# Kernel optimization log

Hardware: AMD Instinct MI355X
Metric: run time of the kernel (lower is better)

The kernel has to match this reference:

```python
import jax, jax.numpy as jnp
import numpy as np

TEMPERATURE = 0.1  # init kwarg
EPS = 1e-8        # torch cosine_similarity eps


def setup_inputs() -> dict:
    key = jax.random.key(0)
    k1, k2, k3 = jax.random.split(key, 3)
    B, D, C = 4096, 1024, 32
    representations = jax.random.normal(k1, (B, D), dtype=jnp.float32)
    soft_labels = jax.random.uniform(k2, (B, C), dtype=jnp.float32)
    labels = jax.random.randint(k3, (B,), 0, 32, dtype=jnp.int64)
    return {
        "representations": representations,
        "soft_labels": soft_labels,
        "labels": labels,
        "pseudo_weight": 10,
    }


def reference(representations, soft_labels, labels, pseudo_weight):
    B = representations.shape[0]
    # row-normalize (cosine similarity)
    norms = jnp.maximum(jnp.linalg.norm(representations, axis=1, keepdims=True), EPS)
    rn = representations / norms
    Z = (rn @ rn.T) / TEMPERATURE                      # [B, B] scaled cosine sims
    E = jnp.exp(Z)
    off_diag = 1.0 - jnp.eye(B, dtype=Z.dtype)         # exclude j == i
    denom = jnp.sum(E * off_diag, axis=1, keepdims=True)   # [B, 1]
    loss_arr = -(Z - jnp.log(denom))                   # -log(exp(Z_ij)/denom_i)
    # positive-pair weights: same label, j != i (detached in original)
    pos = (labels[:, None] == labels[None, :]).astype(Z.dtype) * off_diag
    soft_sim = jax.lax.stop_gradient(soft_labels @ soft_labels.T)  # torch.inner, detached
    w = pos + pseudo_weight * soft_sim
    return jnp.sum(loss_arr * w) / B
```

## Files before the change

kernel.cpp:

```cpp
#include <hip/hip_runtime.h>
#include <hip/hip_bf16.h>
#include <stdint.h>


typedef float f32x4 __attribute__((ext_vector_type(4)));
typedef long i64;

#define INV_T 10.0f
#define Z_SCALE (INV_T / 256.0f)

#define CHUNK_STRIDE 262144

#define GLD16(gp, lp)                                                          \
    __builtin_amdgcn_global_load_lds(                                          \
        (const __attribute__((address_space(1))) uint32_t*)(gp),               \
        (__attribute__((address_space(3))) uint32_t*)(lp), 16, 0, 0)

#define OFF_RNF8  0
#define OFF_DENOM 4194304
#define OFF_POSS  (OFF_DENOM + 16384)
#define OFF_G     (OFF_POSS + 16384)
#define OFF_OACC  (OFF_G + 131072)
#define OFF_DONE  (OFF_OACC + 16)
#define ZERO_SPAN 167936
#define OFF_CSP   (OFF_DENOM + ZERO_SPAN)
#define OFF_CCP   (OFF_CSP + 4096)
#define OFF_W     (OFF_CCP + 4096)

#define N_GEMM 528
#define N_G    512
#define N_W    16

__global__ __launch_bounds__(256) void scl_stage1(const float* __restrict__ rep,
                                                  const float* __restrict__ sl,
                                                  const int* __restrict__ labels,
                                                  uint8_t* __restrict__ rnf8,
                                                  float* __restrict__ cs_part,
                                                  int* __restrict__ cc_part,
                                                  char* __restrict__ zbase) {
    int b = blockIdx.x;
    int t = threadIdx.x;
    if (b < 4096) {
        int row = b;
        const float4* src = reinterpret_cast<const float4*>(rep + (size_t)row * 1024);
        float4 v = src[t];
        float s = v.x * v.x + v.y * v.y + v.z * v.z + v.w * v.w;
#pragma unroll
        for (int m = 1; m < 64; m <<= 1) s += __shfl_xor(s, m, 64);
        __shared__ float red[4];
        if ((t & 63) == 0) red[t >> 6] = s;
        __syncthreads();
        s = red[0] + red[1] + red[2] + red[3];
        float nf = 16.0f / fmaxf(sqrtf(s), 1e-8f);
        int p = 0;
        p = __builtin_amdgcn_cvt_pk_fp8_f32(v.x * nf, v.y * nf, p, false);
        p = __builtin_amdgcn_cvt_pk_fp8_f32(v.z * nf, v.w * nf, p, true);
        *(uint32_t*)&rnf8[(size_t)(t >> 4) * CHUNK_STRIDE + row * 64 + (t & 15) * 4] =
            (uint32_t)p;
    } else if (b < 4128) {
        __shared__ float part[8][32];
        __shared__ int bins[32];
        int bb = b - 4096;
        if (t < 32) bins[t] = 0;
        __syncthreads();
        if (t < 128) atomicAdd(&bins[labels[bb * 128 + t]], 1);
        int c = t & 31, rg = t >> 5;
        float s = 0.f;
#pragma unroll 4
        for (int k = 0; k < 16; ++k) {
            int i = bb * 128 + rg * 16 + k;
            s += sl[i * 32 + c];
        }
        part[rg][c] = s;
        __syncthreads();
        if (t < 32) {
            float tot = 0.f;
#pragma unroll
            for (int g = 0; g < 8; ++g) tot += part[g][t];
            cs_part[bb * 32 + t] = tot;
            cc_part[bb * 32 + t] = bins[t];
        }
    } else {
        int zb = b - 4128;
        *(uint4*)(zbase + (size_t)zb * 4096 + t * 16) = (uint4){0, 0, 0, 0};
    }
}

__global__ __launch_bounds__(256) void scl_gw(const uint8_t* __restrict__ rnf8,
                                              const float* __restrict__ sl,
                                              const int* __restrict__ labels,
                                              const float* __restrict__ cs_part,
                                              const int* __restrict__ cc_part,
                                              const int* __restrict__ pwp,
                                              float* __restrict__ G,
                                              float* __restrict__ W) {
    int tid = threadIdx.x;
    int bIdx = blockIdx.x;

    if (bIdx < N_G) {
        __shared__ __align__(16) uint8_t rns[128 * 64];
        __shared__ __align__(16) float sls[128 * 32];
        int dblk = bIdx & 15, ks = bIdx >> 4;
        int i0 = ks * 128;
        const uint8_t* slab = rnf8 + (size_t)dblk * CHUNK_STRIDE + (size_t)i0 * 64;
#pragma unroll
        for (int p = 0; p < 2; ++p) {
            int off = p * 4096 + tid * 16;
            *(uint4*)&rns[off] = *(const uint4*)&slab[off];
        }
#pragma unroll
        for (int p = 0; p < 4; ++p) {
            int off = p * 1024 + tid * 4;
            *(float4*)&sls[off] = *(const float4*)&sl[(size_t)i0 * 32 + off];
        }
        __syncthreads();
        int dq = tid >> 5, c = tid & 31;
        int d0 = dblk * 64 + dq * 8;
        float acc[8];
#pragma unroll
        for (int j = 0; j < 8; ++j) acc[j] = 0.f;
#pragma unroll 4
        for (int k = 0; k < 128; ++k) {
            uint2 rv = *(const uint2*)&rns[k * 64 + dq * 8];
            float sv = sls[k * 32 + c];
            acc[0] += __builtin_amdgcn_cvt_f32_fp8((int)rv.x, 0) * sv;
            acc[1] += __builtin_amdgcn_cvt_f32_fp8((int)rv.x, 1) * sv;
            acc[2] += __builtin_amdgcn_cvt_f32_fp8((int)rv.x, 2) * sv;
            acc[3] += __builtin_amdgcn_cvt_f32_fp8((int)rv.x, 3) * sv;
            acc[4] += __builtin_amdgcn_cvt_f32_fp8((int)rv.y, 0) * sv;
            acc[5] += __builtin_amdgcn_cvt_f32_fp8((int)rv.y, 1) * sv;
            acc[6] += __builtin_amdgcn_cvt_f32_fp8((int)rv.y, 2) * sv;
            acc[7] += __builtin_amdgcn_cvt_f32_fp8((int)rv.y, 3) * sv;
        }
#pragma unroll
        for (int j = 0; j < 8; ++j)
            atomicAdd(&G[(d0 + j) * 32 + c], acc[j] * 0.0625f);
    } else {
        __shared__ __align__(16) float css[32];
        __shared__ int ccs[32];
        if (tid < 32) {
            float s = 0.f; int n = 0;
#pragma unroll
            for (int b = 0; b < 32; ++b) { s += cs_part[b * 32 + tid]; n += cc_part[b * 32 + tid]; }
            css[tid] = s; ccs[tid] = n;
        }
        __syncthreads();
        int bits = *pwp;
        float pw = (bits >= -(1 << 22) && bits <= (1 << 22)) ? (float)bits
                                                             : __int_as_float(bits);
        int i = (bIdx - N_G) * 256 + tid;
        const f32x4* sl4 = (const f32x4*)sl;
        const f32x4* cs4 = (const f32x4*)css;
        float dW = 0.f;
#pragma unroll
        for (int q = 0; q < 8; ++q) {
            f32x4 s = sl4[i * 8 + q];
            f32x4 c = cs4[q];
            dW += s[0] * c[0] + s[1] * c[1] + s[2] * c[2] + s[3] * c[3];
        }
        W[i] = (float)(ccs[labels[i]] - 1) + pw * dW;
    }
}

__global__ __launch_bounds__(256) void scl_gemm(const uint8_t* __restrict__ rnf8,
                                                const int* __restrict__ labels,
                                                float* __restrict__ denom,
                                                float* __restrict__ posS) {
    int tid = threadIdx.x;
    int bIdx = blockIdx.x;

    __shared__ __align__(16) uint8_t As[3][128 * 64];
    __shared__ __align__(16) uint8_t Bs[3][128 * 64];
    __shared__ int lblA[128], lblB[128];

    int L = (bIdx & 7) * 66 + (bIdx >> 3);
    int bi = 0, rem = L;
    while (rem >= 32 - bi) { rem -= 32 - bi; ++bi; }
    int bj = bi + rem;
    int rowA0 = bi * 128, colB0 = bj * 128;

    if (tid < 128) {
        lblA[tid] = labels[rowA0 + tid];
        lblB[tid] = labels[colB0 + tid];
    }

    int lane = tid & 63, warp = tid >> 6;
    int wr = warp >> 1, wc = warp & 1;
    int m_ = lane & 15, g = lane >> 4;

    int r4 = lane >> 2;
    int csw = (lane & 3) ^ ((lane >> 3) & 3);
    const uint8_t* gA0 = rnf8 + (size_t)(rowA0 + warp * 32 + r4) * 64 + csw * 16;
    const uint8_t* gB0 = rnf8 + (size_t)(colB0 + warp * 32 + r4) * 64 + csw * 16;

    f32x4 acc[4][4];
#pragma unroll
    for (int a = 0; a < 4; ++a)
#pragma unroll
        for (int b = 0; b < 4; ++b) acc[a][b] = (f32x4){0.f, 0.f, 0.f, 0.f};

    int fsw = (g ^ ((m_ >> 1) & 3)) * 16;

    GLD16(gA0,                     &As[0][(warp * 32) * 64]);
    GLD16(gA0 + 1024,              &As[0][(warp * 32 + 16) * 64]);
    GLD16(gB0,                     &Bs[0][(warp * 32) * 64]);
    GLD16(gB0 + 1024,              &Bs[0][(warp * 32 + 16) * 64]);
    GLD16(gA0 + CHUNK_STRIDE,        &As[1][(warp * 32) * 64]);
    GLD16(gA0 + CHUNK_STRIDE + 1024, &As[1][(warp * 32 + 16) * 64]);
    GLD16(gB0 + CHUNK_STRIDE,        &Bs[1][(warp * 32) * 64]);
    GLD16(gB0 + CHUNK_STRIDE + 1024, &Bs[1][(warp * 32 + 16) * 64]);

    asm volatile("s_waitcnt lgkmcnt(0)" ::: "memory");

    for (int kt = 0; kt < 15; ++kt) {
        int cur = kt % 3;
        asm volatile("s_waitcnt vmcnt(4)" ::: "memory");
        __builtin_amdgcn_s_barrier();
        __builtin_amdgcn_sched_barrier(0);
        f32x4 aq[4], bq[4];
#pragma unroll
        for (int ti = 0; ti < 4; ++ti) {
            int rowLoc = wr * 64 + ti * 16 + m_;
            aq[ti] = *(const f32x4*)&As[cur][rowLoc * 64 + fsw];
        }
#pragma unroll
        for (int tj = 0; tj < 4; ++tj) {
            int colLoc = wc * 64 + tj * 16 + m_;
            bq[tj] = *(const f32x4*)&Bs[cur][colLoc * 64 + fsw];
        }
        if (kt < 14) {
            int nxt = (kt + 2) % 3;
            size_t co = (size_t)(kt + 2) * CHUNK_STRIDE;
            GLD16(gA0 + co,        &As[nxt][(warp * 32) * 64]);
            GLD16(gA0 + co + 1024, &As[nxt][(warp * 32 + 16) * 64]);
            GLD16(gB0 + co,        &Bs[nxt][(warp * 32) * 64]);
            GLD16(gB0 + co + 1024, &Bs[nxt][(warp * 32 + 16) * 64]);
        }
#pragma unroll
        for (int s = 0; s < 2; ++s)
#pragma unroll
            for (int ti = 0; ti < 4; ++ti)
#pragma unroll
                for (int tj = 0; tj < 4; ++tj) {
                    i64 a = ((const i64*)&aq[ti])[s];
                    i64 b = ((const i64*)&bq[tj])[s];
                    acc[ti][tj] = __builtin_amdgcn_mfma_f32_16x16x32_fp8_fp8(
                        a, b, acc[ti][tj], 0, 0, 0);
                }
    }
    {
        int cur = 15 % 3;
        asm volatile("s_waitcnt vmcnt(0)" ::: "memory");
        __builtin_amdgcn_s_barrier();
        __builtin_amdgcn_sched_barrier(0);
        f32x4 aq[4], bq[4];
#pragma unroll
        for (int ti = 0; ti < 4; ++ti) {
            int rowLoc = wr * 64 + ti * 16 + m_;
            aq[ti] = *(const f32x4*)&As[cur][rowLoc * 64 + fsw];
        }
#pragma unroll
        for (int tj = 0; tj < 4; ++tj) {
            int colLoc = wc * 64 + tj * 16 + m_;
            bq[tj] = *(const f32x4*)&Bs[cur][colLoc * 64 + fsw];
        }
#pragma unroll
        for (int s = 0; s < 2; ++s)
#pragma unroll
            for (int ti = 0; ti < 4; ++ti)
#pragma unroll
                for (int tj = 0; tj < 4; ++tj) {
                    i64 a = ((const i64*)&aq[ti])[s];
                    i64 b = ((const i64*)&bq[tj])[s];
                    acc[ti][tj] = __builtin_amdgcn_mfma_f32_16x16x32_fp8_fp8(
                        a, b, acc[ti][tj], 0, 0, 0);
                }
    }

    bool isDiag = (bi == bj);
    int cl = m_;
    float colE[4] = {0.f, 0.f, 0.f, 0.f}, colP[4] = {0.f, 0.f, 0.f, 0.f};
#pragma unroll
    for (int ti = 0; ti < 4; ++ti) {
        int rowLoc = wr * 64 + ti * 16 + g * 4;
        float rE[4] = {0.f, 0.f, 0.f, 0.f}, rP[4] = {0.f, 0.f, 0.f, 0.f};
        int lr[4];
#pragma unroll
        for (int r = 0; r < 4; ++r) lr[r] = lblA[rowLoc + r];
#pragma unroll
        for (int tj = 0; tj < 4; ++tj) {
            int colLoc = wc * 64 + tj * 16 + cl;
            int gCol = colB0 + colLoc;
            int lc = lblB[colLoc];
            f32x4 a = acc[ti][tj];
#pragma unroll
            for (int r = 0; r < 4; ++r) {
                int gRow = rowA0 + rowLoc + r;
                float z = Z_SCALE * a[r];
                float e = __expf(z);
                bool offd = (gRow != gCol);
                if (!offd) e = 0.f;
                rE[r] += e;
                colE[tj] += e;
                if (offd && (lr[r] == lc)) { rP[r] += z; colP[tj] += z; }
            }
        }
#pragma unroll
        for (int r = 0; r < 4; ++r) {
            float v = rE[r], p = rP[r];
#pragma unroll
            for (int msk = 1; msk < 16; msk <<= 1) {
                v += __shfl_xor(v, msk, 64);
                p += __shfl_xor(p, msk, 64);
            }
            if (cl == 0) {
                int gRow = rowA0 + rowLoc + r;
                atomicAdd(&denom[gRow], v);
                atomicAdd(&posS[gRow], p);
            }
        }
    }
    if (!isDiag) {
#pragma unroll
        for (int tj = 0; tj < 4; ++tj) {
            float v = colE[tj], p = colP[tj];
            v += __shfl_xor(v, 16, 64); p += __shfl_xor(p, 16, 64);
            v += __shfl_xor(v, 32, 64); p += __shfl_xor(p, 32, 64);
            if (g == 0) {
                int gCol = colB0 + wc * 64 + tj * 16 + cl;
                atomicAdd(&denom[gCol], v);
                atomicAdd(&posS[gCol], p);
            }
        }
    }
}

__global__ __launch_bounds__(256) void scl_finalize(const float* __restrict__ denom,
                                                    const float* __restrict__ posS,
                                                    const float* __restrict__ W,
                                                    const float* __restrict__ G,
                                                    const int* __restrict__ pwp,
                                                    double* __restrict__ oacc,
                                                    int* __restrict__ done,
                                                    float* __restrict__ out) {
    int t = threadIdx.x;
    __shared__ double wsum[4];
    double contrib = 0.0;

    if (blockIdx.x < 8) {
        int i0 = blockIdx.x * 512 + t;
        float t0 = __logf(denom[i0]) * W[i0] - posS[i0];
        float t1 = __logf(denom[i0 + 256]) * W[i0 + 256] - posS[i0 + 256];
        double td = (double)t0 + (double)t1;
#pragma unroll
        for (int m = 1; m < 64; m <<= 1) td += __shfl_xor(td, m, 64);
        if ((t & 63) == 0) wsum[t >> 6] = td;
        __syncthreads();
        contrib = wsum[0] + wsum[1] + wsum[2] + wsum[3];
    } else {
        int bits = *pwp;
        float pw = (bits >= -(1 << 22) && bits <= (1 << 22)) ? (float)bits
                                                             : __int_as_float(bits);
        const f32x4* G4 = (const f32x4*)G;
        float gs = 0.f;
#pragma unroll
        for (int q = 0; q < 32; ++q) {
            f32x4 v = G4[q * 256 + t];
            gs += v[0] * v[0] + v[1] * v[1] + v[2] * v[2] + v[3] * v[3];
        }
        double gd = (double)gs;
#pragma unroll
        for (int m = 1; m < 64; m <<= 1) gd += __shfl_xor(gd, m, 64);
        if ((t & 63) == 0) wsum[t >> 6] = gd;
        __syncthreads();
        contrib = -(double)(pw * INV_T) * (wsum[0] + wsum[1] + wsum[2] + wsum[3]);
    }

    if (t == 0) {
        atomicAdd(oacc, contrib);
        __threadfence();
        int old = atomicAdd(done, 1);
        if (old == 8) {
            double tot = atomicAdd(oacc, 0.0);
            out[0] = (float)(tot * (1.0 / 4096.0));
        }
    }
}

extern "C" void kernel_launch(void* const* d_in, const int* in_sizes, int n_in,
                              void* d_out, int out_size, void* d_ws, size_t ws_size,
                              hipStream_t stream) {
    const float* rep = (const float*)d_in[0];
    const float* sl = (const float*)d_in[1];
    const int* labels = (const int*)d_in[2];
    const int* pwp = (const int*)d_in[3];

    char* ws = (char*)d_ws;
    uint8_t* rnf8 = (uint8_t*)(ws + OFF_RNF8);
    float* denom = (float*)(ws + OFF_DENOM);
    float* posS = (float*)(ws + OFF_POSS);
    float* G = (float*)(ws + OFF_G);
    double* oacc = (double*)(ws + OFF_OACC);
    int* done = (int*)(ws + OFF_DONE);
    float* cs_part = (float*)(ws + OFF_CSP);
    int* cc_part = (int*)(ws + OFF_CCP);
    float* W = (float*)(ws + OFF_W);

    scl_stage1<<<4169, 256, 0, stream>>>(rep, sl, labels, rnf8,
                                         cs_part, cc_part, ws + OFF_DENOM);
    scl_gw<<<N_G + N_W, 256, 0, stream>>>(rnf8, sl, labels, cs_part, cc_part,
                                          pwp, G, W);
    scl_gemm<<<N_GEMM, 256, 0, stream>>>(rnf8, labels, denom, posS);
    scl_finalize<<<9, 256, 0, stream>>>(denom, posS, W, G, pwp, oacc, done,
                                        (float*)d_out);
}
```

Baseline: 117.8 us.

## Load GEMM fragments directly from global into registers, dropping LDS staging

The triple-buffered LDS pipeline (global_load_lds plus barriers) is replaced by direct per-lane 16-byte global loads into MFMA fragment registers, double-buffered in registers across K chunks. This removes LDS traffic and block-level barriers from the main loop. Each wave now fetches its own A/B rows, so global and L2 traffic rises because tiles are no longer shared across waves. Register pressure also grows from the two fragment sets.

```diff
diff --git a/kernel.cpp b/kernel.cpp
--- a/kernel.cpp
+++ b/kernel.cpp
@@ -10,11 +10,6 @@
 #define Z_SCALE (INV_T / 256.0f)
 
 #define CHUNK_STRIDE 262144
-
-#define GLD16(gp, lp)                                                          \
-    __builtin_amdgcn_global_load_lds(                                          \
-        (const __attribute__((address_space(1))) uint32_t*)(gp),               \
-        (__attribute__((address_space(3))) uint32_t*)(lp), 16, 0, 0)
 
 #define OFF_RNF8  0
 #define OFF_DENOM 4194304
@@ -169,8 +164,6 @@
     int tid = threadIdx.x;
     int bIdx = blockIdx.x;
 
-    __shared__ __align__(16) uint8_t As[3][128 * 64];
-    __shared__ __align__(16) uint8_t Bs[3][128 * 64];
     __shared__ int lblA[128], lblB[128];
 
     int L = (bIdx & 7) * 66 + (bIdx >> 3);
@@ -183,15 +176,14 @@
         lblA[tid] = labels[rowA0 + tid];
         lblB[tid] = labels[colB0 + tid];
     }
+    __syncthreads();
 
     int lane = tid & 63, warp = tid >> 6;
     int wr = warp >> 1, wc = warp & 1;
     int m_ = lane & 15, g = lane >> 4;
 
-    int r4 = lane >> 2;
-    int csw = (lane & 3) ^ ((lane >> 3) & 3);
-    const uint8_t* gA0 = rnf8 + (size_t)(rowA0 + warp * 32 + r4) * 64 + csw * 16;
-    const uint8_t* gB0 = rnf8 + (size_t)(colB0 + warp * 32 + r4) * 64 + csw * 16;
+    const uint8_t* gAf = rnf8 + (size_t)(rowA0 + wr * 64 + m_) * 64 + g * 16;
+    const uint8_t* gBf = rnf8 + (size_t)(colB0 + wc * 64 + m_) * 64 + g * 16;
 
     f32x4 acc[4][4];
 #pragma unroll
@@ -199,83 +191,42 @@
 #pragma unroll
         for (int b = 0; b < 4; ++b) acc[a][b] = (f32x4){0.f, 0.f, 0.f, 0.f};
 
-    int fsw = (g ^ ((m_ >> 1) & 3)) * 16;
-
-    GLD16(gA0,                     &As[0][(warp * 32) * 64]);
-    GLD16(gA0 + 1024,              &As[0][(warp * 32 + 16) * 64]);
-    GLD16(gB0,                     &Bs[0][(warp * 32) * 64]);
-    GLD16(gB0 + 1024,              &Bs[0][(warp * 32 + 16) * 64]);
-    GLD16(gA0 + CHUNK_STRIDE,        &As[1][(warp * 32) * 64]);
-    GLD16(gA0 + CHUNK_STRIDE + 1024, &As[1][(warp * 32 + 16) * 64]);
-    GLD16(gB0 + CHUNK_STRIDE,        &Bs[1][(warp * 32) * 64]);
-    GLD16(gB0 + CHUNK_STRIDE + 1024, &Bs[1][(warp * 32 + 16) * 64]);
-
-    asm volatile("s_waitcnt lgkmcnt(0)" ::: "memory");
-
-    for (int kt = 0; kt < 15; ++kt) {
-        int cur = kt % 3;
-        asm volatile("s_waitcnt vmcnt(4)" ::: "memory");
-        __builtin_amdgcn_s_barrier();
-        __builtin_amdgcn_sched_barrier(0);
-        f32x4 aq[4], bq[4];
-#pragma unroll
-        for (int ti = 0; ti < 4; ++ti) {
-            int rowLoc = wr * 64 + ti * 16 + m_;
-            aq[ti] = *(const f32x4*)&As[cur][rowLoc * 64 + fsw];
-        }
-#pragma unroll
-        for (int tj = 0; tj < 4; ++tj) {
-            int colLoc = wc * 64 + tj * 16 + m_;
-            bq[tj] = *(const f32x4*)&Bs[cur][colLoc * 64 + fsw];
-        }
-        if (kt < 14) {
-            int nxt = (kt + 2) % 3;
-            size_t co = (size_t)(kt + 2) * CHUNK_STRIDE;
-            GLD16(gA0 + co,        &As[nxt][(warp * 32) * 64]);
-            GLD16(gA0 + co + 1024, &As[nxt][(warp * 32 + 16) * 64]);
-            GLD16(gB0 + co,        &Bs[nxt][(warp * 32) * 64]);
-            GLD16(gB0 + co + 1024, &Bs[nxt][(warp * 32 + 16) * 64]);
-        }
-#pragma unroll
-        for (int s = 0; s < 2; ++s)
-#pragma unroll
-            for (int ti = 0; ti < 4; ++ti)
-#pragma unroll
-                for (int tj = 0; tj < 4; ++tj) {
-                    i64 a = ((const i64*)&aq[ti])[s];
-                    i64 b = ((const i64*)&bq[tj])[s];
-                    acc[ti][tj] = __builtin_amdgcn_mfma_f32_16x16x32_fp8_fp8(
-                        a, b, acc[ti][tj], 0, 0, 0);
-                }
-    }
-    {
-        int cur = 15 % 3;
-        asm volatile("s_waitcnt vmcnt(0)" ::: "memory");
-        __builtin_amdgcn_s_barrier();
-        __builtin_amdgcn_sched_barrier(0);
-        f32x4 aq[4], bq[4];
-#pragma unroll
-        for (int ti = 0; ti < 4; ++ti) {
-            int rowLoc = wr * 64 + ti * 16 + m_;
-            aq[ti] = *(const f32x4*)&As[cur][rowLoc * 64 + fsw];
-        }
-#pragma unroll
-        for (int tj = 0; tj < 4; ++tj) {
-            int colLoc = wc * 64 + tj * 16 + m_;
-            bq[tj] = *(const f32x4*)&Bs[cur][colLoc * 64 + fsw];
-        }
-#pragma unroll
-        for (int s = 0; s < 2; ++s)
-#pragma unroll
-            for (int ti = 0; ti < 4; ++ti)
-#pragma unroll
-                for (int tj = 0; tj < 4; ++tj) {
-                    i64 a = ((const i64*)&aq[ti])[s];
-                    i64 b = ((const i64*)&bq[tj])[s];
-                    acc[ti][tj] = __builtin_amdgcn_mfma_f32_16x16x32_fp8_fp8(
-                        a, b, acc[ti][tj], 0, 0, 0);
-                }
-    }
+    f32x4 a0[4], b0[4], a1[4], b1[4];
+
+#define MFMA_SET(AF, BF)                                                       \
+    _Pragma("unroll") for (int s = 0; s < 2; ++s)                              \
+        _Pragma("unroll") for (int ti = 0; ti < 4; ++ti)                       \
+            _Pragma("unroll") for (int tj = 0; tj < 4; ++tj) {                 \
+                i64 av = ((const i64*)&AF[ti])[s];                             \
+                i64 bv = ((const i64*)&BF[tj])[s];                             \
+                acc[ti][tj] = __builtin_amdgcn_mfma_f32_16x16x32_fp8_fp8(      \
+                    av, bv, acc[ti][tj], 0, 0, 0);                             \
+            }
+
+#pragma unroll
+    for (int t = 0; t < 4; ++t) {
+        a0[t] = *(const f32x4*)(gAf + t * 1024);
+        b0[t] = *(const f32x4*)(gBf + t * 1024);
+    }
+    for (int kt = 0; kt < 16; kt += 2) {
+        size_t c1 = (size_t)(kt + 1) * CHUNK_STRIDE;
+#pragma unroll
+        for (int t = 0; t < 4; ++t) {
+            a1[t] = *(const f32x4*)(gAf + c1 + t * 1024);
+            b1[t] = *(const f32x4*)(gBf + c1 + t * 1024);
+        }
+        MFMA_SET(a0, b0);
+        if (kt + 2 < 16) {
+            size_t c2 = (size_t)(kt + 2) * CHUNK_STRIDE;
+#pragma unroll
+            for (int t = 0; t < 4; ++t) {
+                a0[t] = *(const f32x4*)(gAf + c2 + t * 1024);
+                b0[t] = *(const f32x4*)(gBf + c2 + t * 1024);
+            }
+        }
+        MFMA_SET(a1, b1);
+    }
+#undef MFMA_SET
 
     bool isDiag = (bi == bj);
     int cl = m_;
```

Result: slower. 124.0 us (+5.3%).
